# Kernel tuning notes

Measured on AMD Instinct MI355X. Metric: run time of the kernel, lower is better.

Reference implementation:

```python
import jax, jax.numpy as jnp
import numpy as np

B, T, C, J = 2048, 128, 3, 25   # batch, frames, coords, joints
E = 64                          # structure elements (n_elements)


def setup_inputs() -> dict:
    key = jax.random.key(0)
    k1, k2 = jax.random.split(key)
    x = jax.random.normal(k1, (B, T, C, J), dtype=jnp.float32)
    centres = jax.random.uniform(k2, (E, 2), dtype=jnp.float32)
    sharpness = jnp.full((E, 2), 3.0, dtype=jnp.float32)  # torch init: ones*3
    return {"x": x, "centres": centres, "sharpness": sharpness}


def _mst_deaths(Dm):
    """Prim's MST over dense distance matrix Dm [n,n].
    The multiset of MST edge weights equals the finite death times of the
    0-dim Vietoris-Rips persistence diagram (births are all 0)."""
    n = Dm.shape[0]
    in_tree0 = jnp.zeros(n, dtype=bool).at[0].set(True)

    def step(carry, _):
        mind, in_tree = carry
        masked = jnp.where(in_tree, jnp.inf, mind)  # distance from tree to each node
        j = jnp.argmin(masked)
        w = masked[j]                               # weight of edge added to MST
        in_tree = in_tree.at[j].set(True)
        mind = jnp.minimum(mind, Dm[j])
        return (mind, in_tree), w

    (_, _), deaths = jax.lax.scan(step, (Dm[0], in_tree0), None, length=n - 1)
    return deaths  # [n-1]


def reference(x, centres, sharpness):
    # --- dense preprocessing ---
    h = x.mean(1)                           # [B, C, J]
    h = h[..., :, None] - h[..., None, :]   # [B, C, J, J] pairwise coord diffs
    h = h.mean(-3)                          # [B, J, J]
    h = jnp.sqrt((h * h).sum(axis=1))       # torch.norm(., 2, dim=1) -> [B, J]
    lo, hi = h.min(), h.max()
    rng = hi - lo
    safe = rng > 1e-8
    h = jnp.where(safe, (h - lo) / jnp.where(safe, rng, 1.0), jnp.zeros_like(h))

    # --- Vietoris-Rips dim-0 persistence on point cloud h: B points in J dims ---
    sq = (h * h).sum(-1)
    d2 = sq[:, None] + sq[None, :] - 2.0 * (h @ h.T)       # [B, B]
    Dm = jnp.sqrt(jnp.maximum(d2, 1e-12))
    deaths = _mst_deaths(Dm)                               # [B-1]
    pd = jnp.stack([jnp.zeros_like(deaths), deaths], -1)[None]  # [1, P, 2]

    # --- StructureElementLayer: out[b,e] = sum_p exp(-sum_d s[e,d]^2 (pd-c)^2) ---
    s2 = sharpness * sharpness                             # [E, 2]
    diff = pd[:, :, None, :] - centres[None, None, :, :]   # [1, P, E, 2]
    out = jnp.exp(-(diff * diff * s2).sum(-1)).sum(1)      # [1, E]
    return out
```

## Files before the change

### kernel.cpp

```cpp
#include <hip/hip_runtime.h>
#include <math.h>

#define B_N 2048
#define T_N 128
#define C_N 3
#define J_N 25
#define E_N 64
#define TC  (T_N*C_N)
#define TCJ (TC*J_N)
#define NQ4 (TCJ/4)

#define D_OFF      0
#define H_OFF      (B_N*B_N)
#define BLO_OFF    (H_OFF + B_N*J_N)
#define BHI_OFF    (BLO_OFF + B_N)
#define COMP_OFF   (BHI_OFF + B_N)
#define CNT_OFF    (COMP_OFF + B_N)
#define DEATHS_OFF (CNT_OFF + 2)
#define BEST_OFF   (DEATHS_OFF + B_N)

typedef unsigned long long u64;
#define U64MAX 0xFFFFFFFFFFFFFFFFull

__global__ void __launch_bounds__(256) k_reduce(const float* __restrict__ x,
                                                float* __restrict__ ws) {
    __shared__ float4 part[250];
    __shared__ float S[100];
    __shared__ float Mj[25];
    const int t = threadIdx.x, b = blockIdx.x;
    if (t == 0) {
        ((unsigned*)(ws + COMP_OFF))[b] = (unsigned)b;
        if (b == 0) *(unsigned*)(ws + CNT_OFF) = 0u;
    }
    const float4* x4 = (const float4*)(x + (size_t)b * TCJ);
    if (t < 250) {
        float4 a; a.x = a.y = a.z = a.w = 0.f;
        for (int idx = t; idx < NQ4; idx += 250) {
            float4 v = x4[idx];
            a.x += v.x; a.y += v.y; a.z += v.z; a.w += v.w;
        }
        part[t] = a;
    }
    __syncthreads();
    if (t < 25) {
        float4 s = part[t];
        #pragma unroll
        for (int g = 1; g < 10; ++g) {
            float4 v = part[t + 25 * g];
            s.x += v.x; s.y += v.y; s.z += v.z; s.w += v.w;
        }
        S[4*t] = s.x; S[4*t+1] = s.y; S[4*t+2] = s.z; S[4*t+3] = s.w;
    }
    __syncthreads();
    if (t < 25) Mj[t] = (S[t] + S[t+25] + S[t+50] + S[t+75]) * (1.0f / 384.0f);
    __syncthreads();
    if (t < 25) {
        float mj = Mj[t], acc = 0.f;
        #pragma unroll
        for (int i = 0; i < J_N; ++i) { float d = Mj[i] - mj; acc += d * d; }
        float hv = sqrtf(acc);
        ws[H_OFF + b * J_N + t] = hv;
        S[t] = hv;
    }
    __syncthreads();
    if (t == 0) {
        float lo = S[0], hi = S[0];
        #pragma unroll
        for (int i = 1; i < J_N; ++i) { lo = fminf(lo, S[i]); hi = fmaxf(hi, S[i]); }
        ws[BLO_OFF + b] = lo;
        ws[BHI_OFF + b] = hi;
    }
}

__global__ void k_dist(float* ws) {
    __shared__ float A[16][26], Bsh[16][26];
    const int tx = threadIdx.x, ty = threadIdx.y;
    const int flat = ty * 16 + tx;
    const int rowA = blockIdx.x * 16, rowB = blockIdx.y * 16;
    const float* h = ws + H_OFF;
    for (int idx = flat; idx < 16 * J_N; idx += 256) {
        int r = idx / J_N, c = idx % J_N;
        A[r][c]   = h[(rowA + r) * J_N + c];
        Bsh[r][c] = h[(rowB + r) * J_N + c];
    }
    __syncthreads();
    float acc = 0.f;
    #pragma unroll
    for (int k = 0; k < J_N; ++k) {
        float d = A[ty][k] - Bsh[tx][k];
        acc += d * d;
    }
    float* D = ws + D_OFF;
    D[(size_t)(rowA + ty) * B_N + rowB + tx] = sqrtf(fmaxf(acc, 1e-12f));
}

__global__ void __launch_bounds__(1024) k_scan(float* __restrict__ ws) {
    if (*(const unsigned*)(ws + CNT_OFF) >= B_N - 1) return;
    const int t = threadIdx.x, w = t >> 6, lane = t & 63;
    const int row = blockIdx.x * 16 + w;
    const unsigned* comp = (const unsigned*)(ws + COMP_OFF);
    const unsigned ci = comp[row];
    const float4* row4 = (const float4*)(ws + D_OFF + (size_t)row * B_N);
    const uint4* comp4 = (const uint4*)comp;
    u64 best = U64MAX;
    #pragma unroll
    for (int k = 0; k < 8; ++k) {
        const int q = k * 64 + lane;
        float4 w4 = row4[q];
        uint4  c4 = comp4[q];
        const unsigned j0 = (unsigned)(q * 4);
        float wv[4] = {w4.x, w4.y, w4.z, w4.w};
        unsigned cv[4] = {c4.x, c4.y, c4.z, c4.w};
        #pragma unroll
        for (int m = 0; m < 4; ++m) {
            if (cv[m] != ci) {
                unsigned j = j0 + m;
                unsigned a = min((unsigned)row, j), b2 = max((unsigned)row, j);
                u64 key = ((u64)__float_as_uint(wv[m]) << 32) | (a << 11) | b2;
                if (key < best) best = key;
            }
        }
    }
    #pragma unroll
    for (int off = 32; off; off >>= 1) {
        u64 o = __shfl_down(best, off);
        if (o < best) best = o;
    }
    if (lane == 0) ((u64*)(ws + BEST_OFF))[row] = best;
}

__global__ void __launch_bounds__(1024) k_union(float* __restrict__ ws) {
    unsigned* gcnt = (unsigned*)(ws + CNT_OFF);
    const unsigned base = *gcnt;
    if (base >= B_N - 1) return;
    __shared__ u64 cb[B_N];
    __shared__ unsigned par[B_N];
    __shared__ unsigned cnt_s;
    unsigned* comp = (unsigned*)(ws + COMP_OFF);
    const u64* best = (const u64*)(ws + BEST_OFF);
    float* deaths = ws + DEATHS_OFF;
    const int t = threadIdx.x;
    if (t == 0) cnt_s = 0u;
    cb[t] = U64MAX; cb[t + 1024] = U64MAX;
    __syncthreads();
    #pragma unroll
    for (int i = t; i < B_N; i += 1024) {
        u64 bkey = best[i];
        if (bkey != U64MAX) atomicMin(&cb[comp[i]], bkey);
    }
    __syncthreads();
    #pragma unroll
    for (int c = t; c < B_N; c += 1024) {
        u64 k = cb[c];
        unsigned p = (unsigned)c;
        if (k != U64MAX) {
            unsigned a  = (unsigned)((k >> 11) & 0x7FFu);
            unsigned b2 = (unsigned)(k & 0x7FFu);
            unsigned ca = comp[a], cbv = comp[b2];
            unsigned c2 = (ca == (unsigned)c) ? cbv : ca;
            p = c2;
            if (!(cb[c2] == k && c2 < (unsigned)c)) {
                unsigned li = atomicAdd(&cnt_s, 1u);
                deaths[base + li] = __uint_as_float((unsigned)(k >> 32));
            }
        }
        par[c] = p;
    }
    __syncthreads();
    #pragma unroll
    for (int c = t; c < B_N; c += 1024) {
        unsigned p = par[c];
        if (p != (unsigned)c && par[p] == (unsigned)c && (unsigned)c < p) par[c] = (unsigned)c;
    }
    __syncthreads();
    for (int it = 0; it < 11; ++it) {
        unsigned np0 = par[par[t]];
        unsigned np1 = par[par[t + 1024]];
        __syncthreads();
        par[t] = np0;
        par[t + 1024] = np1;
        __syncthreads();
    }
    #pragma unroll
    for (int i = t; i < B_N; i += 1024) comp[i] = par[comp[i]];
    if (t == 0) *gcnt = base + cnt_s;
}

__global__ void __launch_bounds__(256) k_struct(const float* __restrict__ ws,
                                                const float* __restrict__ centres,
                                                const float* __restrict__ sharp,
                                                float* __restrict__ out) {
    const int e = blockIdx.x, t = threadIdx.x;
    const int lane = t & 63, wv = t >> 6;
    __shared__ float red[8];
    __shared__ float wsum[4];
    float lo = INFINITY, hi = -INFINITY;
    #pragma unroll
    for (int k = 0; k < 8; ++k) {
        int i = k * 256 + t;
        lo = fminf(lo, ws[BLO_OFF + i]);
        hi = fmaxf(hi, ws[BHI_OFF + i]);
    }
    #pragma unroll
    for (int off = 32; off; off >>= 1) {
        lo = fminf(lo, __shfl_down(lo, off));
        hi = fmaxf(hi, __shfl_down(hi, off));
    }
    if (lane == 0) { red[wv] = lo; red[wv + 4] = hi; }
    __syncthreads();
    lo = fminf(fminf(red[0], red[1]), fminf(red[2], red[3]));
    hi = fmaxf(fmaxf(red[4], red[5]), fmaxf(red[6], red[7]));
    float rng = hi - lo;
    float rinv = (rng > 1e-8f) ? 1.0f / rng : 0.0f;

    const float* deaths = ws + DEATHS_OFF;
    const float c0 = centres[e * 2], c1 = centres[e * 2 + 1];
    const float s0 = sharp[e * 2],   s1 = sharp[e * 2 + 1];
    const float s1sq = s1 * s1;
    float acc = 0.f;
    for (int p = t; p < B_N - 1; p += 256) {
        float d = deaths[p] * rinv - c1;
        acc += expf(-s1sq * d * d);
    }
    #pragma unroll
    for (int off = 32; off; off >>= 1) acc += __shfl_down(acc, off);
    if (lane == 0) wsum[wv] = acc;
    __syncthreads();
    if (t == 0) {
        float tot = wsum[0] + wsum[1] + wsum[2] + wsum[3];
        out[e] = expf(-s0 * s0 * c0 * c0) * tot;
    }
}

extern "C" void kernel_launch(void* const* d_in, const int* in_sizes, int n_in,
                              void* d_out, int out_size, void* d_ws, size_t ws_size,
                              hipStream_t stream) {
    const float* x       = (const float*)d_in[0];
    const float* centres = (const float*)d_in[1];
    const float* sharp   = (const float*)d_in[2];
    float* out = (float*)d_out;
    float* ws  = (float*)d_ws;

    hipLaunchKernelGGL(k_reduce, dim3(B_N),      dim3(256),    0, stream, x, ws);
    hipLaunchKernelGGL(k_dist,   dim3(128, 128), dim3(16, 16), 0, stream, ws);
    for (int r = 0; r < 11; ++r) {
        hipLaunchKernelGGL(k_scan,  dim3(128), dim3(1024), 0, stream, ws);
        hipLaunchKernelGGL(k_union, dim3(1),   dim3(1024), 0, stream, ws);
    }
    hipLaunchKernelGGL(k_struct, dim3(E_N), dim3(256), 0, stream, ws, centres, sharp, out);
}
```

Before: 196.1 us.

## Fuse Boruvka rounds and structure layer into one cooperative persistent kernel

Replaces the 22 alternating scan/union launches and the final structure-element launch with one cooperative kernel of 256 blocks that loops over the Boruvka rounds using grid.sync. Every block keeps its own copy of the component array in shared memory and repeats the union step redundantly, so the global union kernel and its round trips through global memory go away. Best-edge buffers alternate between two slots so that one round's reads do not race with the next round's writes. The cost is redundant union work in every block, reliance on grid-wide barriers, and cooperative launch limits on how many blocks can be co-resident.

Result: slower. 274.1 us (+39.8%).

```diff
diff --git a/kernel.cpp b/kernel.cpp
--- a/kernel.cpp
+++ b/kernel.cpp
@@ -1,5 +1,8 @@
 #include <hip/hip_runtime.h>
+#include <hip/hip_cooperative_groups.h>
 #include <math.h>
+
+namespace cg = cooperative_groups;
 
 #define B_N 2048
 #define T_N 128
@@ -14,9 +17,7 @@
 #define H_OFF      (B_N*B_N)
 #define BLO_OFF    (H_OFF + B_N*J_N)
 #define BHI_OFF    (BLO_OFF + B_N)
-#define COMP_OFF   (BHI_OFF + B_N)
-#define CNT_OFF    (COMP_OFF + B_N)
-#define DEATHS_OFF (CNT_OFF + 2)
+#define DEATHS_OFF (BHI_OFF + B_N)
 #define BEST_OFF   (DEATHS_OFF + B_N)
 
 typedef unsigned long long u64;
@@ -28,10 +29,6 @@
     __shared__ float S[100];
     __shared__ float Mj[25];
     const int t = threadIdx.x, b = blockIdx.x;
-    if (t == 0) {
-        ((unsigned*)(ws + COMP_OFF))[b] = (unsigned)b;
-        if (b == 0) *(unsigned*)(ws + CNT_OFF) = 0u;
-    }
     const float4* x4 = (const float4*)(x + (size_t)b * TCJ);
     if (t < 250) {
         float4 a; a.x = a.y = a.z = a.w = 0.f;
@@ -94,140 +91,149 @@
     D[(size_t)(rowA + ty) * B_N + rowB + tx] = sqrtf(fmaxf(acc, 1e-12f));
 }
 
-__global__ void __launch_bounds__(1024) k_scan(float* __restrict__ ws) {
-    if (*(const unsigned*)(ws + CNT_OFF) >= B_N - 1) return;
-    const int t = threadIdx.x, w = t >> 6, lane = t & 63;
-    const int row = blockIdx.x * 16 + w;
-    const unsigned* comp = (const unsigned*)(ws + COMP_OFF);
-    const unsigned ci = comp[row];
-    const float4* row4 = (const float4*)(ws + D_OFF + (size_t)row * B_N);
-    const uint4* comp4 = (const uint4*)comp;
-    u64 best = U64MAX;
-    #pragma unroll
-    for (int k = 0; k < 8; ++k) {
-        const int q = k * 64 + lane;
-        float4 w4 = row4[q];
-        uint4  c4 = comp4[q];
-        const unsigned j0 = (unsigned)(q * 4);
-        float wv[4] = {w4.x, w4.y, w4.z, w4.w};
-        unsigned cv[4] = {c4.x, c4.y, c4.z, c4.w};
-        #pragma unroll
-        for (int m = 0; m < 4; ++m) {
-            if (cv[m] != ci) {
-                unsigned j = j0 + m;
-                unsigned a = min((unsigned)row, j), b2 = max((unsigned)row, j);
-                u64 key = ((u64)__float_as_uint(wv[m]) << 32) | (a << 11) | b2;
-                if (key < best) best = key;
-            }
-        }
-    }
-    #pragma unroll
-    for (int off = 32; off; off >>= 1) {
-        u64 o = __shfl_down(best, off);
-        if (o < best) best = o;
-    }
-    if (lane == 0) ((u64*)(ws + BEST_OFF))[row] = best;
-}
-
-__global__ void __launch_bounds__(1024) k_union(float* __restrict__ ws) {
-    unsigned* gcnt = (unsigned*)(ws + CNT_OFF);
-    const unsigned base = *gcnt;
-    if (base >= B_N - 1) return;
+__global__ void __launch_bounds__(1024) k_mst(float* __restrict__ ws,
+                                              const float* __restrict__ centres,
+                                              const float* __restrict__ sharp,
+                                              float* __restrict__ out) {
+    cg::grid_group grid = cg::this_grid();
+    __shared__ __align__(16) unsigned comp[B_N];
     __shared__ u64 cb[B_N];
     __shared__ unsigned par[B_N];
+    __shared__ u64 sc[16];
     __shared__ unsigned cnt_s;
-    unsigned* comp = (unsigned*)(ws + COMP_OFF);
-    const u64* best = (const u64*)(ws + BEST_OFF);
+    const int t = threadIdx.x, blk = blockIdx.x;
+    const int w = t >> 6, lane = t & 63;
+    const float* D = ws + D_OFF;
     float* deaths = ws + DEATHS_OFF;
-    const int t = threadIdx.x;
-    if (t == 0) cnt_s = 0u;
-    cb[t] = U64MAX; cb[t + 1024] = U64MAX;
-    __syncthreads();
-    #pragma unroll
-    for (int i = t; i < B_N; i += 1024) {
-        u64 bkey = best[i];
-        if (bkey != U64MAX) atomicMin(&cb[comp[i]], bkey);
-    }
-    __syncthreads();
-    #pragma unroll
-    for (int c = t; c < B_N; c += 1024) {
-        u64 k = cb[c];
-        unsigned p = (unsigned)c;
-        if (k != U64MAX) {
-            unsigned a  = (unsigned)((k >> 11) & 0x7FFu);
-            unsigned b2 = (unsigned)(k & 0x7FFu);
-            unsigned ca = comp[a], cbv = comp[b2];
-            unsigned c2 = (ca == (unsigned)c) ? cbv : ca;
-            p = c2;
-            if (!(cb[c2] == k && c2 < (unsigned)c)) {
-                unsigned li = atomicAdd(&cnt_s, 1u);
-                deaths[base + li] = __uint_as_float((unsigned)(k >> 32));
+    u64* bestbuf[2] = { (u64*)(ws + BEST_OFF), (u64*)(ws + BEST_OFF) + B_N };
+
+    comp[t] = (unsigned)t;
+    comp[t + 1024] = (unsigned)(t + 1024);
+    __syncthreads();
+
+    unsigned base = 0;
+    for (int r = 0; r < 11; ++r) {
+        u64* bbuf = bestbuf[r & 1];
+        const int row = blk * 8 + (w >> 1);
+        const int half = w & 1;
+        const unsigned ci = comp[row];
+        const float4* row4 = (const float4*)(D + (size_t)row * B_N);
+        const uint4* comp4 = (const uint4*)comp;
+        u64 bst = U64MAX;
+        #pragma unroll
+        for (int k = 0; k < 4; ++k) {
+            const int q = half * 256 + k * 64 + lane;
+            float4 w4 = row4[q];
+            uint4  c4 = comp4[q];
+            const unsigned j0 = (unsigned)(q * 4);
+            float wv[4] = {w4.x, w4.y, w4.z, w4.w};
+            unsigned cv[4] = {c4.x, c4.y, c4.z, c4.w};
+            #pragma unroll
+            for (int m = 0; m < 4; ++m) {
+                if (cv[m] != ci) {
+                    unsigned j = j0 + m;
+                    unsigned a = min((unsigned)row, j), b2 = max((unsigned)row, j);
+                    u64 key = ((u64)__float_as_uint(wv[m]) << 32) | (a << 11) | b2;
+                    if (key < bst) bst = key;
+                }
             }
         }
-        par[c] = p;
-    }
-    __syncthreads();
-    #pragma unroll
-    for (int c = t; c < B_N; c += 1024) {
-        unsigned p = par[c];
-        if (p != (unsigned)c && par[p] == (unsigned)c && (unsigned)c < p) par[c] = (unsigned)c;
-    }
-    __syncthreads();
-    for (int it = 0; it < 11; ++it) {
-        unsigned np0 = par[par[t]];
-        unsigned np1 = par[par[t + 1024]];
-        __syncthreads();
-        par[t] = np0;
-        par[t + 1024] = np1;
-        __syncthreads();
-    }
-    #pragma unroll
-    for (int i = t; i < B_N; i += 1024) comp[i] = par[comp[i]];
-    if (t == 0) *gcnt = base + cnt_s;
-}
-
-__global__ void __launch_bounds__(256) k_struct(const float* __restrict__ ws,
-                                                const float* __restrict__ centres,
-                                                const float* __restrict__ sharp,
-                                                float* __restrict__ out) {
-    const int e = blockIdx.x, t = threadIdx.x;
-    const int lane = t & 63, wv = t >> 6;
-    __shared__ float red[8];
-    __shared__ float wsum[4];
-    float lo = INFINITY, hi = -INFINITY;
-    #pragma unroll
-    for (int k = 0; k < 8; ++k) {
-        int i = k * 256 + t;
-        lo = fminf(lo, ws[BLO_OFF + i]);
-        hi = fmaxf(hi, ws[BHI_OFF + i]);
-    }
+        #pragma unroll
+        for (int off = 32; off; off >>= 1) {
+            u64 o = __shfl_down(bst, off);
+            if (o < bst) bst = o;
+        }
+        if (lane == 0) sc[w] = bst;
+        __syncthreads();
+        if (lane == 0 && half == 0) {
+            u64 a = sc[w], b2 = sc[w | 1];
+            bbuf[row] = (a < b2) ? a : b2;
+        }
+        grid.sync();
+
+        if (t == 0) cnt_s = 0u;
+        cb[t] = U64MAX; cb[t + 1024] = U64MAX;
+        __syncthreads();
+        #pragma unroll
+        for (int i = t; i < B_N; i += 1024) {
+            u64 bk = bbuf[i];
+            if (bk != U64MAX) atomicMin(&cb[comp[i]], bk);
+        }
+        __syncthreads();
+        #pragma unroll
+        for (int c = t; c < B_N; c += 1024) {
+            u64 k = cb[c];
+            unsigned p = (unsigned)c;
+            if (k != U64MAX) {
+                unsigned a  = (unsigned)((k >> 11) & 0x7FFu);
+                unsigned b2 = (unsigned)(k & 0x7FFu);
+                unsigned ca = comp[a], cbv = comp[b2];
+                unsigned c2 = (ca == (unsigned)c) ? cbv : ca;
+                p = c2;
+                if (!(cb[c2] == k && c2 < (unsigned)c)) {
+                    unsigned li = atomicAdd(&cnt_s, 1u);
+                    if (blk == 0) deaths[base + li] = __uint_as_float((unsigned)(k >> 32));
+                }
+            }
+            par[c] = p;
+        }
+        __syncthreads();
+        #pragma unroll
+        for (int c = t; c < B_N; c += 1024) {
+            unsigned p = par[c];
+            if (p != (unsigned)c && par[p] == (unsigned)c && (unsigned)c < p) par[c] = (unsigned)c;
+        }
+        __syncthreads();
+        for (int it = 0; it < 11; ++it) {
+            unsigned n0 = par[par[t]];
+            unsigned n1 = par[par[t + 1024]];
+            __syncthreads();
+            par[t] = n0;
+            par[t + 1024] = n1;
+            __syncthreads();
+        }
+        #pragma unroll
+        for (int i = t; i < B_N; i += 1024) comp[i] = par[comp[i]];
+        __syncthreads();
+        base += cnt_s;
+        if (base >= B_N - 1) break;
+    }
+    grid.sync();
+
+    if (blk >= E_N) return;
+    __shared__ float redlo[16], redhi[16], wsum[16];
+    float lo = fminf(ws[BLO_OFF + t], ws[BLO_OFF + t + 1024]);
+    float hi = fmaxf(ws[BHI_OFF + t], ws[BHI_OFF + t + 1024]);
     #pragma unroll
     for (int off = 32; off; off >>= 1) {
         lo = fminf(lo, __shfl_down(lo, off));
         hi = fmaxf(hi, __shfl_down(hi, off));
     }
-    if (lane == 0) { red[wv] = lo; red[wv + 4] = hi; }
-    __syncthreads();
-    lo = fminf(fminf(red[0], red[1]), fminf(red[2], red[3]));
-    hi = fmaxf(fmaxf(red[4], red[5]), fmaxf(red[6], red[7]));
+    if (lane == 0) { redlo[w] = lo; redhi[w] = hi; }
+    __syncthreads();
+    lo = redlo[0]; hi = redhi[0];
+    #pragma unroll
+    for (int k = 1; k < 16; ++k) { lo = fminf(lo, redlo[k]); hi = fmaxf(hi, redhi[k]); }
     float rng = hi - lo;
     float rinv = (rng > 1e-8f) ? 1.0f / rng : 0.0f;
 
-    const float* deaths = ws + DEATHS_OFF;
+    const int e = blk;
     const float c0 = centres[e * 2], c1 = centres[e * 2 + 1];
     const float s0 = sharp[e * 2],   s1 = sharp[e * 2 + 1];
     const float s1sq = s1 * s1;
     float acc = 0.f;
-    for (int p = t; p < B_N - 1; p += 256) {
+    for (int p = t; p < B_N - 1; p += 1024) {
         float d = deaths[p] * rinv - c1;
         acc += expf(-s1sq * d * d);
     }
     #pragma unroll
     for (int off = 32; off; off >>= 1) acc += __shfl_down(acc, off);
-    if (lane == 0) wsum[wv] = acc;
+    if (lane == 0) wsum[w] = acc;
     __syncthreads();
     if (t == 0) {
-        float tot = wsum[0] + wsum[1] + wsum[2] + wsum[3];
+        float tot = 0.f;
+        #pragma unroll
+        for (int k = 0; k < 16; ++k) tot += wsum[k];
         out[e] = expf(-s0 * s0 * c0 * c0) * tot;
     }
 }
@@ -243,9 +249,7 @@
 
     hipLaunchKernelGGL(k_reduce, dim3(B_N),      dim3(256),    0, stream, x, ws);
     hipLaunchKernelGGL(k_dist,   dim3(128, 128), dim3(16, 16), 0, stream, ws);
-    for (int r = 0; r < 11; ++r) {
-        hipLaunchKernelGGL(k_scan,  dim3(128), dim3(1024), 0, stream, ws);
-        hipLaunchKernelGGL(k_union, dim3(1),   dim3(1024), 0, stream, ws);
-    }
-    hipLaunchKernelGGL(k_struct, dim3(E_N), dim3(256), 0, stream, ws, centres, sharp, out);
-}
+
+    void* args[] = { (void*)&ws, (void*)&centres, (void*)&sharp, (void*)&out };
+    hipLaunchCooperativeKernel((void*)k_mst, dim3(256), dim3(1024), args, 0, stream);
+}
```

## Fuse Boruvka union step into scan blocks redundantly to halve launches

Applied to the files above, without the earlier changes.

Every one of the 128 scan blocks now repeats the single-block union/contraction step in shared memory and then runs its own min-edge scan, with component arrays and best-edge buffers double-buffered by parity. This removes the alternating single-block union launches and the serial gaps between them, cutting the chain from 22 launches to 11. The final union round and the structure-element layer are merged into one kernel, pointer jumping is replaced by root chasing, and the first scan skips the component check. The price is 128-fold redundant union work and extra global traffic to copy the component array into every block.

New measurement: 191.6 us. 2.3% less time.

```diff
diff --git a/kernel.cpp b/kernel.cpp
--- a/kernel.cpp
+++ b/kernel.cpp
@@ -14,10 +14,10 @@
 #define H_OFF      (B_N*B_N)
 #define BLO_OFF    (H_OFF + B_N*J_N)
 #define BHI_OFF    (BLO_OFF + B_N)
-#define COMP_OFF   (BHI_OFF + B_N)
-#define CNT_OFF    (COMP_OFF + B_N)
-#define DEATHS_OFF (CNT_OFF + 2)
+#define DEATHS_OFF (BHI_OFF + B_N)
 #define BEST_OFF   (DEATHS_OFF + B_N)
+#define COMP_OFF   (BEST_OFF + 4*B_N)
+#define GC_OFF     (COMP_OFF + 2*B_N)
 
 typedef unsigned long long u64;
 #define U64MAX 0xFFFFFFFFFFFFFFFFull
@@ -28,10 +28,6 @@
     __shared__ float S[100];
     __shared__ float Mj[25];
     const int t = threadIdx.x, b = blockIdx.x;
-    if (t == 0) {
-        ((unsigned*)(ws + COMP_OFF))[b] = (unsigned)b;
-        if (b == 0) *(unsigned*)(ws + CNT_OFF) = 0u;
-    }
     const float4* x4 = (const float4*)(x + (size_t)b * TCJ);
     if (t < 250) {
         float4 a; a.x = a.y = a.z = a.w = 0.f;
@@ -94,27 +90,21 @@
     D[(size_t)(rowA + ty) * B_N + rowB + tx] = sqrtf(fmaxf(acc, 1e-12f));
 }
 
-__global__ void __launch_bounds__(1024) k_scan(float* __restrict__ ws) {
-    if (*(const unsigned*)(ws + CNT_OFF) >= B_N - 1) return;
+__global__ void __launch_bounds__(1024) k_scan0(float* __restrict__ ws) {
     const int t = threadIdx.x, w = t >> 6, lane = t & 63;
     const int row = blockIdx.x * 16 + w;
-    const unsigned* comp = (const unsigned*)(ws + COMP_OFF);
-    const unsigned ci = comp[row];
     const float4* row4 = (const float4*)(ws + D_OFF + (size_t)row * B_N);
-    const uint4* comp4 = (const uint4*)comp;
     u64 best = U64MAX;
     #pragma unroll
     for (int k = 0; k < 8; ++k) {
         const int q = k * 64 + lane;
         float4 w4 = row4[q];
-        uint4  c4 = comp4[q];
         const unsigned j0 = (unsigned)(q * 4);
         float wv[4] = {w4.x, w4.y, w4.z, w4.w};
-        unsigned cv[4] = {c4.x, c4.y, c4.z, c4.w};
         #pragma unroll
         for (int m = 0; m < 4; ++m) {
-            if (cv[m] != ci) {
-                unsigned j = j0 + m;
+            unsigned j = j0 + m;
+            if (j != (unsigned)row) {
                 unsigned a = min((unsigned)row, j), b2 = max((unsigned)row, j);
                 u64 key = ((u64)__float_as_uint(wv[m]) << 32) | (a << 11) | b2;
                 if (key < best) best = key;
@@ -127,26 +117,36 @@
         if (o < best) best = o;
     }
     if (lane == 0) ((u64*)(ws + BEST_OFF))[row] = best;
-}
-
-__global__ void __launch_bounds__(1024) k_union(float* __restrict__ ws) {
-    unsigned* gcnt = (unsigned*)(ws + CNT_OFF);
-    const unsigned base = *gcnt;
+    if (blockIdx.x == 0) {
+        unsigned* gc = (unsigned*)(ws + COMP_OFF);
+        gc[t] = (unsigned)t; gc[t + 1024] = (unsigned)(t + 1024);
+        if (t == 0) { ((unsigned*)(ws + GC_OFF))[0] = 0u; ((unsigned*)(ws + GC_OFF))[1] = 0u; }
+    }
+}
+
+__global__ void __launch_bounds__(1024) k_round(float* __restrict__ ws, int par_in) {
+    unsigned* gcnt = (unsigned*)(ws + GC_OFF);
+    const unsigned base = gcnt[par_in];
     if (base >= B_N - 1) return;
+    __shared__ __align__(16) unsigned comp[B_N];
     __shared__ u64 cb[B_N];
     __shared__ unsigned par[B_N];
     __shared__ unsigned cnt_s;
-    unsigned* comp = (unsigned*)(ws + COMP_OFF);
-    const u64* best = (const u64*)(ws + BEST_OFF);
+    const int t = threadIdx.x, blk = blockIdx.x;
+    const unsigned* gcomp_in = (const unsigned*)(ws + COMP_OFF) + par_in * B_N;
+    unsigned* gcomp_out = (unsigned*)(ws + COMP_OFF) + (par_in ^ 1) * B_N;
+    const u64* bin = (const u64*)(ws + BEST_OFF) + par_in * B_N;
+    u64* bout = (u64*)(ws + BEST_OFF) + (par_in ^ 1) * B_N;
     float* deaths = ws + DEATHS_OFF;
-    const int t = threadIdx.x;
+
     if (t == 0) cnt_s = 0u;
+    comp[t] = gcomp_in[t]; comp[t + 1024] = gcomp_in[t + 1024];
     cb[t] = U64MAX; cb[t + 1024] = U64MAX;
     __syncthreads();
     #pragma unroll
     for (int i = t; i < B_N; i += 1024) {
-        u64 bkey = best[i];
-        if (bkey != U64MAX) atomicMin(&cb[comp[i]], bkey);
+        u64 bk = bin[i];
+        if (bk != U64MAX) atomicMin(&cb[comp[i]], bk);
     }
     __syncthreads();
     #pragma unroll
@@ -161,7 +161,7 @@
             p = c2;
             if (!(cb[c2] == k && c2 < (unsigned)c)) {
                 unsigned li = atomicAdd(&cnt_s, 1u);
-                deaths[base + li] = __uint_as_float((unsigned)(k >> 32));
+                if (blk == 0) deaths[base + li] = __uint_as_float((unsigned)(k >> 32));
             }
         }
         par[c] = p;
@@ -173,31 +173,102 @@
         if (p != (unsigned)c && par[p] == (unsigned)c && (unsigned)c < p) par[c] = (unsigned)c;
     }
     __syncthreads();
-    for (int it = 0; it < 11; ++it) {
-        unsigned np0 = par[par[t]];
-        unsigned np1 = par[par[t + 1024]];
-        __syncthreads();
-        par[t] = np0;
-        par[t + 1024] = np1;
-        __syncthreads();
-    }
+    #pragma unroll
+    for (int c = t; c < B_N; c += 1024) {
+        unsigned r = par[c];
+        while (true) { unsigned pr = par[r]; if (pr == r) break; r = pr; }
+        par[c] = r;
+    }
+    __syncthreads();
     #pragma unroll
     for (int i = t; i < B_N; i += 1024) comp[i] = par[comp[i]];
-    if (t == 0) *gcnt = base + cnt_s;
-}
-
-__global__ void __launch_bounds__(256) k_struct(const float* __restrict__ ws,
+    __syncthreads();
+    const unsigned newbase = base + cnt_s;
+    const bool conv = (newbase >= B_N - 1);
+    if (blk == 0) {
+        gcomp_out[t] = comp[t]; gcomp_out[t + 1024] = comp[t + 1024];
+        if (t == 0) { gcnt[par_in ^ 1] = newbase; if (conv) gcnt[par_in] = newbase; }
+    }
+    if (conv) return;
+
+    const int w = t >> 6, lane = t & 63;
+    const int row = blk * 16 + w;
+    const unsigned ci = comp[row];
+    const float4* row4 = (const float4*)(ws + D_OFF + (size_t)row * B_N);
+    const uint4* comp4 = (const uint4*)comp;
+    u64 best = U64MAX;
+    #pragma unroll
+    for (int k = 0; k < 8; ++k) {
+        const int q = k * 64 + lane;
+        float4 w4 = row4[q];
+        uint4  c4 = comp4[q];
+        const unsigned j0 = (unsigned)(q * 4);
+        float wv[4] = {w4.x, w4.y, w4.z, w4.w};
+        unsigned cv[4] = {c4.x, c4.y, c4.z, c4.w};
+        #pragma unroll
+        for (int m = 0; m < 4; ++m) {
+            if (cv[m] != ci) {
+                unsigned j = j0 + m;
+                unsigned a = min((unsigned)row, j), b2 = max((unsigned)row, j);
+                u64 key = ((u64)__float_as_uint(wv[m]) << 32) | (a << 11) | b2;
+                if (key < best) best = key;
+            }
+        }
+    }
+    #pragma unroll
+    for (int off = 32; off; off >>= 1) {
+        u64 o = __shfl_down(best, off);
+        if (o < best) best = o;
+    }
+    if (lane == 0) bout[row] = best;
+}
+
+__global__ void __launch_bounds__(1024) k_final(float* __restrict__ ws,
                                                 const float* __restrict__ centres,
                                                 const float* __restrict__ sharp,
                                                 float* __restrict__ out) {
-    const int e = blockIdx.x, t = threadIdx.x;
-    const int lane = t & 63, wv = t >> 6;
-    __shared__ float red[8];
-    __shared__ float wsum[4];
+    __shared__ __align__(16) unsigned comp[B_N];
+    __shared__ u64 cb[B_N];
+    __shared__ unsigned par[B_N];
+    __shared__ unsigned cnt_s;
+    __shared__ float redlo[16], redhi[16];
+    const int t = threadIdx.x;
+    unsigned* gcnt = (unsigned*)(ws + GC_OFF);
+    float* deaths = ws + DEATHS_OFF;
+    const unsigned base = gcnt[0];
+    if (base < B_N - 1) {
+        const unsigned* gcomp_in = (const unsigned*)(ws + COMP_OFF);
+        const u64* bin = (const u64*)(ws + BEST_OFF);
+        if (t == 0) cnt_s = 0u;
+        comp[t] = gcomp_in[t]; comp[t + 1024] = gcomp_in[t + 1024];
+        cb[t] = U64MAX; cb[t + 1024] = U64MAX;
+        __syncthreads();
+        #pragma unroll
+        for (int i = t; i < B_N; i += 1024) {
+            u64 bk = bin[i];
+            if (bk != U64MAX) atomicMin(&cb[comp[i]], bk);
+        }
+        __syncthreads();
+        #pragma unroll
+        for (int c = t; c < B_N; c += 1024) {
+            u64 k = cb[c];
+            if (k != U64MAX) {
+                unsigned a  = (unsigned)((k >> 11) & 0x7FFu);
+                unsigned b2 = (unsigned)(k & 0x7FFu);
+                unsigned ca = comp[a], cbv = comp[b2];
+                unsigned c2 = (ca == (unsigned)c) ? cbv : ca;
+                if (!(cb[c2] == k && c2 < (unsigned)c)) {
+                    unsigned li = atomicAdd(&cnt_s, 1u);
+                    deaths[base + li] = __uint_as_float((unsigned)(k >> 32));
+                }
+            }
+        }
+        __syncthreads();
+    }
+    const int w = t >> 6, lane = t & 63;
     float lo = INFINITY, hi = -INFINITY;
     #pragma unroll
-    for (int k = 0; k < 8; ++k) {
-        int i = k * 256 + t;
+    for (int i = t; i < B_N; i += 1024) {
         lo = fminf(lo, ws[BLO_OFF + i]);
         hi = fmaxf(hi, ws[BHI_OFF + i]);
     }
@@ -206,29 +277,26 @@
         lo = fminf(lo, __shfl_down(lo, off));
         hi = fmaxf(hi, __shfl_down(hi, off));
     }
-    if (lane == 0) { red[wv] = lo; red[wv + 4] = hi; }
-    __syncthreads();
-    lo = fminf(fminf(red[0], red[1]), fminf(red[2], red[3]));
-    hi = fmaxf(fmaxf(red[4], red[5]), fmaxf(red[6], red[7]));
+    if (lane == 0) { redlo[w] = lo; redhi[w] = hi; }
+    __syncthreads();
+    lo = redlo[0]; hi = redhi[0];
+    #pragma unroll
+    for (int k = 1; k < 16; ++k) { lo = fminf(lo, redlo[k]); hi = fmaxf(hi, redhi[k]); }
     float rng = hi - lo;
     float rinv = (rng > 1e-8f) ? 1.0f / rng : 0.0f;
 
-    const float* deaths = ws + DEATHS_OFF;
-    const float c0 = centres[e * 2], c1 = centres[e * 2 + 1];
-    const float s0 = sharp[e * 2],   s1 = sharp[e * 2 + 1];
-    const float s1sq = s1 * s1;
-    float acc = 0.f;
-    for (int p = t; p < B_N - 1; p += 256) {
-        float d = deaths[p] * rinv - c1;
-        acc += expf(-s1sq * d * d);
-    }
-    #pragma unroll
-    for (int off = 32; off; off >>= 1) acc += __shfl_down(acc, off);
-    if (lane == 0) wsum[wv] = acc;
-    __syncthreads();
-    if (t == 0) {
-        float tot = wsum[0] + wsum[1] + wsum[2] + wsum[3];
-        out[e] = expf(-s0 * s0 * c0 * c0) * tot;
+    for (int e = w; e < E_N; e += 16) {
+        const float c0 = centres[e * 2], c1 = centres[e * 2 + 1];
+        const float s0 = sharp[e * 2],   s1 = sharp[e * 2 + 1];
+        const float s1sq = s1 * s1;
+        float acc = 0.f;
+        for (int p = lane; p < B_N - 1; p += 64) {
+            float d = deaths[p] * rinv - c1;
+            acc += expf(-s1sq * d * d);
+        }
+        #pragma unroll
+        for (int off = 32; off; off >>= 1) acc += __shfl_down(acc, off);
+        if (lane == 0) out[e] = expf(-s0 * s0 * c0 * c0) * acc;
     }
 }
 
@@ -243,9 +311,8 @@
 
     hipLaunchKernelGGL(k_reduce, dim3(B_N),      dim3(256),    0, stream, x, ws);
     hipLaunchKernelGGL(k_dist,   dim3(128, 128), dim3(16, 16), 0, stream, ws);
-    for (int r = 0; r < 11; ++r) {
-        hipLaunchKernelGGL(k_scan,  dim3(128), dim3(1024), 0, stream, ws);
-        hipLaunchKernelGGL(k_union, dim3(1),   dim3(1024), 0, stream, ws);
-    }
-    hipLaunchKernelGGL(k_struct, dim3(E_N), dim3(256), 0, stream, ws, centres, sharp, out);
-}
+    hipLaunchKernelGGL(k_scan0,  dim3(128),      dim3(1024),   0, stream, ws);
+    for (int r = 0; r < 10; ++r)
+        hipLaunchKernelGGL(k_round, dim3(128), dim3(1024), 0, stream, ws, r & 1);
+    hipLaunchKernelGGL(k_final, dim3(1), dim3(1024), 0, stream, ws, centres, sharp, out);
+}
```
